# Kernel optimization log

Measured on AMD Instinct MI355X. Metric: run time of the kernel, lower is better.

## Reference

```python
import jax, jax.numpy as jnp
import numpy as np

TEX_H = 256
TEX_W = 256
F_CH = 16
D_FACTOR = 0.5
DECAY = float(np.sqrt(2.0 * D_FACTOR * D_FACTOR))           # sqrt(d^2 + d^2)
AF = int(-np.log(0.1) * DECAY + 0.5)                        # active_field = 2
K = 2 * AF                                                  # 4x4 splat window


def setup_inputs() -> dict:
    key = jax.random.key(0)
    k1, k2, k3 = jax.random.split(key, 3)
    B, H, W = 8, 256, 256
    f_map = jax.random.normal(k1, (B, H, W, F_CH), dtype=jnp.float32)
    uv_map = jax.random.uniform(k2, (B, H, W, 2), dtype=jnp.float32)   # uv in [0,1)
    mask = (jax.random.uniform(k3, (B, H, W, 1)) < 0.5).astype(jnp.float32)
    return {"f_map": f_map, "uv_map": uv_map, "mask": mask}


def reference(f_map, uv_map, mask):
    B, H, W, C = f_map.shape
    N = B * H * W
    # uv_map[..., ::-1] * [tex_h, tex_w]: v comes from channel 1, u from channel 0
    v = (uv_map[..., 1] * TEX_H).reshape(N)
    u = (uv_map[..., 0] * TEX_W).reshape(N)
    pix = f_map.reshape(N, C)
    m = mask.reshape(N)  # 1 = masked pixel contributes (TF gathers where mask==1)

    v_shift = jnp.maximum(v - AF, 0.0)
    u_shift = jnp.maximum(u - AF, 0.0)
    offs = jnp.arange(K, dtype=jnp.float32)
    v_grid = v_shift[:, None, None] + offs[None, :, None]   # [N,K,K]
    u_grid = u_shift[:, None, None] + offs[None, None, :]   # [N,K,K]

    du = jnp.abs(u_grid - u[:, None, None])
    du = jnp.minimum(du, jnp.abs(du - TEX_W))               # wrap-around distance
    dv = jnp.abs(v_grid - v[:, None, None])
    dv = jnp.minimum(dv, jnp.abs(dv - TEX_H))
    wmap = jnp.exp(-jnp.sqrt(du * du + dv * dv) / DECAY)
    wmap = wmap * (wmap > 0.1) * m[:, None, None]           # threshold + mask gating

    vi = v_grid.astype(jnp.int32)
    ui = u_grid.astype(jnp.int32)
    valid = (vi < TEX_H) & (ui < TEX_W)                     # drop out-of-range splats
    wmap = wmap * valid
    idx = (jnp.clip(vi, 0, TEX_H - 1) * TEX_W + jnp.clip(ui, 0, TEX_W - 1)).reshape(-1)

    w_flat = wmap.reshape(-1)                               # [N*K*K]
    vals = (wmap.reshape(N, K * K)[..., None] * pix[:, None, :]).reshape(-1, C)

    wsum = jnp.zeros((TEX_H * TEX_W,), jnp.float32).at[idx].add(w_flat)
    csum = jnp.zeros((TEX_H * TEX_W, C), jnp.float32).at[idx].add(vals)
    wsum = wsum.reshape(TEX_H, TEX_W, 1)
    csum = csum.reshape(TEX_H, TEX_W, C)

    tex = (csum * (wsum > 0.01)) / (wsum + 0.001)           # weighted average
    return jnp.broadcast_to(tex[None], (B, TEX_H, TEX_W, C))
```

## Files before the change

### kernel.cpp

```cpp
#include <hip/hip_runtime.h>
#include <hip/hip_fp16.h>

#define TEX_H 256
#define TEX_W 256
#define FCH 16
#define NPIX (8 * 256 * 256)
#define NCELL (256 * 256)

#define SQRT2_F 1.41421356237f
#define W_EDGE   0.24311673443f
#define W_DIAG   0.13533528324f

typedef float vf4 __attribute__((ext_vector_type(4)));

#define HALO_H_OFF 0
#define HALO_N_OFF (NCELL * 16 * 2)
#define DIR_C_OFF  (HALO_N_OFF + NCELL * 4)
#define DIR_W_OFF  (DIR_C_OFF + 2048 * 16 * 4)
#define ZERO_BYTES (DIR_W_OFF + 2048 * 4)

__global__ __launch_bounds__(256) void splat_kernel(
    const float*  __restrict__ f_map,
    const float2* __restrict__ uv_map,
    const float*  __restrict__ mask,
    char* __restrict__ wsb)
{
    __half2* halo = (__half2*)(wsb + HALO_H_OFF);
    float*   hcnt = (float*)  (wsb + HALO_N_OFF);
    float*   dirc = (float*)  (wsb + DIR_C_OFF);
    float*   dirw = (float*)  (wsb + DIR_W_OFF);

    int tid = blockIdx.x * 256 + threadIdx.x;
    int pix = tid >> 3;
    int l   = tid & 7;

    if (mask[pix] == 0.0f) return;

    float2 uv = uv_map[pix];
    float u = uv.x * 256.0f;
    float v = uv.y * 256.0f;

    if (u >= 2.0f && v >= 2.0f) {
        int cell = ((int)v) * 256 + (int)u;
        float2 fp = ((const float2*)f_map)[(size_t)pix * 8 + l];
        __half2 h = __floats2half2_rn(fp.x, fp.y);
        unsafeAtomicAdd(&halo[(size_t)cell * 8 + l], h);
        if (l == 0) unsafeAtomicAdd(&hcnt[cell], 1.0f);
    } else {
        float fa = f_map[(size_t)pix * FCH + l];
        float fb = f_map[(size_t)pix * FCH + l + 8];
        float us = fmaxf(u - 2.0f, 0.0f);
        float vs = fmaxf(v - 2.0f, 0.0f);
        #pragma unroll
        for (int kv = 0; kv < 4; ++kv) {
            float vg = vs + (float)kv;
            int vi = (int)vg;
            float dvf = fabsf(vg - v);
            #pragma unroll
            for (int ku = 0; ku < 4; ++ku) {
                float ug = us + (float)ku;
                int ui = (int)ug;
                float duf = fabsf(ug - u);
                float w = expf(-sqrtf(duf * duf + dvf * dvf) * SQRT2_F);
                if (w > 0.1f && vi < TEX_H && ui < TEX_W) {
                    int cell = (ui < 4) ? (ui * 256 + vi)
                                        : ((4 + vi) * 256 + ui);
                    unsafeAtomicAdd(&dirc[(size_t)cell * FCH + l],     w * fa);
                    unsafeAtomicAdd(&dirc[(size_t)cell * FCH + l + 8], w * fb);
                    if (l == 0) unsafeAtomicAdd(&dirw[cell], w);
                }
            }
        }
    }
}

__global__ __launch_bounds__(256) void finalize_kernel(
    const char* __restrict__ wsb,
    float* __restrict__ out)
{
    const __half2* halo = (const __half2*)(wsb + HALO_H_OFF);
    const float*   hcnt = (const float*)  (wsb + HALO_N_OFF);
    const float*   dirc = (const float*)  (wsb + DIR_C_OFF);
    const float*   dirw = (const float*)  (wsb + DIR_W_OFF);

    __shared__ __half2 s_h[100][8];
    __shared__ float   s_n[100];

    int tile = blockIdx.x;
    int r0 = (tile >> 5) << 3;
    int c0 = (tile & 31) << 3;

    int i = threadIdx.x;
    if (i < 200) {
        int cellIdx = i >> 1, part = i & 1;
        int hr = cellIdx / 10, hc = cellIdx - hr * 10;
        int gr = r0 + hr - 1, gc = c0 + hc - 1;
        uint4 val = make_uint4(0, 0, 0, 0);
        bool inb = (gr >= 0) & (gr < 256) & (gc >= 0) & (gc < 256);
        if (inb)
            val = *(const uint4*)&halo[((size_t)gr * 256 + gc) * 8 + part * 4];
        *(uint4*)&s_h[cellIdx][part * 4] = val;
        if (part == 0) s_n[cellIdx] = inb ? hcnt[gr * 256 + gc] : 0.0f;
    }
    __syncthreads();

    int tx = threadIdx.x >> 2;
    int c4 = threadIdx.x & 3;
    int lr = tx >> 3, lc = tx & 7;
    int gr = r0 + lr, gc = c0 + lc;

    vf4 cs = {0.f, 0.f, 0.f, 0.f};
    float wsm = 0.0f;

    #pragma unroll
    for (int a = 0; a < 3; ++a) {
        #pragma unroll
        for (int b = 0; b < 3; ++b) {
            float w = (a == 1 && b == 1) ? 1.0f
                    : ((a == 1 || b == 1) ? W_EDGE : W_DIAG);
            int idx = (lr + a) * 10 + (lc + b);
            float2 f0 = __half22float2(s_h[idx][c4 * 2 + 0]);
            float2 f1 = __half22float2(s_h[idx][c4 * 2 + 1]);
            cs.x += w * f0.x; cs.y += w * f0.y;
            cs.z += w * f1.x; cs.w += w * f1.y;
            wsm  += w * s_n[idx];
        }
    }

    if (gc < 4) {
        int cell = gc * 256 + gr;
        cs += *(const vf4*)&dirc[(size_t)cell * FCH + c4 * 4];
        wsm += dirw[cell];
    } else if (gr < 4) {
        int cell = (4 + gr) * 256 + gc;
        cs += *(const vf4*)&dirc[(size_t)cell * FCH + c4 * 4];
        wsm += dirw[cell];
    }

    float s = (wsm > 0.01f) ? (1.0f / (wsm + 0.001f)) : 0.0f;
    cs *= s;

    size_t base = ((size_t)gr * 256 + gc) * FCH + c4 * 4;
    #pragma unroll
    for (int b = 0; b < 8; ++b) {
        __builtin_nontemporal_store(cs, (vf4*)&out[(size_t)b * (256 * 256 * FCH) + base]);
    }
}

extern "C" void kernel_launch(void* const* d_in, const int* in_sizes, int n_in,
                              void* d_out, int out_size, void* d_ws, size_t ws_size,
                              hipStream_t stream) {
    const float*  f_map  = (const float*)d_in[0];
    const float2* uv_map = (const float2*)d_in[1];
    const float*  mask   = (const float*)d_in[2];
    float* out = (float*)d_out;
    char*  wsb = (char*)d_ws;

    (void)hipMemsetAsync(wsb, 0, (size_t)ZERO_BYTES, stream);

    splat_kernel<<<(NPIX * 8) / 256, 256, 0, stream>>>(f_map, uv_map, mask, wsb);
    finalize_kernel<<<1024, 256, 0, stream>>>(wsb, out);
}
```

Measured before the change: 60.79 us.

## Privatize halo accumulation buffers into replicas to reduce atomic contention

The splat kernel now spreads its interior atomic adds across up to 8 replicated copies of the half-precision halo and count buffers, picking the copy by block index. The finalize kernel sums the replicas while loading the tile halo and stores the result in float shared memory. The aim is to cut contention and serialization on hot texture cells during atomics. In exchange there is a larger memset, more finalize reads, and a runtime loop over replicas.

After: 71.76 us. 18.0% more time.

```diff
diff --git a/kernel.cpp b/kernel.cpp
--- a/kernel.cpp
+++ b/kernel.cpp
@@ -13,23 +13,16 @@
 
 typedef float vf4 __attribute__((ext_vector_type(4)));
 
-#define HALO_H_OFF 0
-#define HALO_N_OFF (NCELL * 16 * 2)
-#define DIR_C_OFF  (HALO_N_OFF + NCELL * 4)
-#define DIR_W_OFF  (DIR_C_OFF + 2048 * 16 * 4)
-#define ZERO_BYTES (DIR_W_OFF + 2048 * 4)
-
 __global__ __launch_bounds__(256) void splat_kernel(
     const float*  __restrict__ f_map,
     const float2* __restrict__ uv_map,
     const float*  __restrict__ mask,
-    char* __restrict__ wsb)
+    __half2* __restrict__ halo,
+    float*   __restrict__ hcnt,
+    float*   __restrict__ dirc,
+    float*   __restrict__ dirw,
+    int repmask)
 {
-    __half2* halo = (__half2*)(wsb + HALO_H_OFF);
-    float*   hcnt = (float*)  (wsb + HALO_N_OFF);
-    float*   dirc = (float*)  (wsb + DIR_C_OFF);
-    float*   dirw = (float*)  (wsb + DIR_W_OFF);
-
     int tid = blockIdx.x * 256 + threadIdx.x;
     int pix = tid >> 3;
     int l   = tid & 7;
@@ -41,10 +34,11 @@
     float v = uv.y * 256.0f;
 
     if (u >= 2.0f && v >= 2.0f) {
-        int cell = ((int)v) * 256 + (int)u;
+        int rep  = blockIdx.x & repmask;
+        size_t cell = (size_t)(rep) * NCELL + ((int)v) * 256 + (int)u;
         float2 fp = ((const float2*)f_map)[(size_t)pix * 8 + l];
         __half2 h = __floats2half2_rn(fp.x, fp.y);
-        unsafeAtomicAdd(&halo[(size_t)cell * 8 + l], h);
+        unsafeAtomicAdd(&halo[cell * 8 + l], h);
         if (l == 0) unsafeAtomicAdd(&hcnt[cell], 1.0f);
     } else {
         float fa = f_map[(size_t)pix * FCH + l];
@@ -75,16 +69,15 @@
 }
 
 __global__ __launch_bounds__(256) void finalize_kernel(
-    const char* __restrict__ wsb,
+    const __half2* __restrict__ halo,
+    const float*   __restrict__ hcnt,
+    const float*   __restrict__ dirc,
+    const float*   __restrict__ dirw,
+    int nrepl,
     float* __restrict__ out)
 {
-    const __half2* halo = (const __half2*)(wsb + HALO_H_OFF);
-    const float*   hcnt = (const float*)  (wsb + HALO_N_OFF);
-    const float*   dirc = (const float*)  (wsb + DIR_C_OFF);
-    const float*   dirw = (const float*)  (wsb + DIR_W_OFF);
-
-    __shared__ __half2 s_h[100][8];
-    __shared__ float   s_n[100];
+    __shared__ float s_h[100][16];
+    __shared__ float s_n[100];
 
     int tile = blockIdx.x;
     int r0 = (tile >> 5) << 3;
@@ -95,12 +88,26 @@
         int cellIdx = i >> 1, part = i & 1;
         int hr = cellIdx / 10, hc = cellIdx - hr * 10;
         int gr = r0 + hr - 1, gc = c0 + hc - 1;
-        uint4 val = make_uint4(0, 0, 0, 0);
         bool inb = (gr >= 0) & (gr < 256) & (gc >= 0) & (gc < 256);
-        if (inb)
-            val = *(const uint4*)&halo[((size_t)gr * 256 + gc) * 8 + part * 4];
-        *(uint4*)&s_h[cellIdx][part * 4] = val;
-        if (part == 0) s_n[cellIdx] = inb ? hcnt[gr * 256 + gc] : 0.0f;
+        float acc[8] = {0,0,0,0,0,0,0,0};
+        float ncc = 0.0f;
+        if (inb) {
+            size_t gcell = (size_t)gr * 256 + gc;
+            for (int r = 0; r < nrepl; ++r) {
+                uint4 val = *(const uint4*)&halo[((size_t)r * NCELL + gcell) * 8 + part * 4];
+                const __half2* hp = (const __half2*)&val;
+                #pragma unroll
+                for (int j = 0; j < 4; ++j) {
+                    float2 f = __half22float2(hp[j]);
+                    acc[j * 2 + 0] += f.x;
+                    acc[j * 2 + 1] += f.y;
+                }
+                if (part == 0) ncc += hcnt[(size_t)r * NCELL + gcell];
+            }
+        }
+        #pragma unroll
+        for (int j = 0; j < 8; ++j) s_h[cellIdx][part * 8 + j] = acc[j];
+        if (part == 0) s_n[cellIdx] = ncc;
     }
     __syncthreads();
 
@@ -119,11 +126,8 @@
             float w = (a == 1 && b == 1) ? 1.0f
                     : ((a == 1 || b == 1) ? W_EDGE : W_DIAG);
             int idx = (lr + a) * 10 + (lc + b);
-            float2 f0 = __half22float2(s_h[idx][c4 * 2 + 0]);
-            float2 f1 = __half22float2(s_h[idx][c4 * 2 + 1]);
-            cs.x += w * f0.x; cs.y += w * f0.y;
-            cs.z += w * f1.x; cs.w += w * f1.y;
-            wsm  += w * s_n[idx];
+            cs += w * *(const vf4*)&s_h[idx][c4 * 4];
+            wsm += w * s_n[idx];
         }
     }
 
@@ -156,8 +160,21 @@
     float* out = (float*)d_out;
     char*  wsb = (char*)d_ws;
 
-    (void)hipMemsetAsync(wsb, 0, (size_t)ZERO_BYTES, stream);
+    const size_t STRIP_BYTES = 2048 * 16 * 4 + 2048 * 4;
+    int nrepl = 8;
+    while (nrepl > 1 &&
+           (size_t)nrepl * NCELL * 36 + STRIP_BYTES > ws_size) nrepl >>= 1;
 
-    splat_kernel<<<(NPIX * 8) / 256, 256, 0, stream>>>(f_map, uv_map, mask, wsb);
-    finalize_kernel<<<1024, 256, 0, stream>>>(wsb, out);
+    size_t halo_bytes = (size_t)nrepl * NCELL * 32;
+    size_t hcnt_bytes = (size_t)nrepl * NCELL * 4;
+    __half2* halo = (__half2*)wsb;
+    float*   hcnt = (float*)(wsb + halo_bytes);
+    float*   dirc = (float*)(wsb + halo_bytes + hcnt_bytes);
+    float*   dirw = (float*)(wsb + halo_bytes + hcnt_bytes + 2048 * 16 * 4);
+
+    (void)hipMemsetAsync(wsb, 0, halo_bytes + hcnt_bytes + STRIP_BYTES, stream);
+
+    splat_kernel<<<(NPIX * 8) / 256, 256, 0, stream>>>(
+        f_map, uv_map, mask, halo, hcnt, dirc, dirw, nrepl - 1);
+    finalize_kernel<<<1024, 256, 0, stream>>>(halo, hcnt, dirc, dirw, nrepl, out);
 }
```
